# Performance work log

Hardware: AMD Instinct MI355X
Metric: run time of the kernel (lower is better)

## Reference

```python
import jax, jax.numpy as jnp
import numpy as np

B, C, H, W = 8, 512, 32, 32
NH = 8
DH = C // NH
HW = H * W
LN_EPS = 1e-5
NORM_EPS = 1e-12  # torch F.normalize eps


def setup_inputs() -> dict:
    key = jax.random.key(0)
    ks = jax.random.split(key, 8)
    s = 0.02
    return {
        "x": jax.random.normal(ks[0], (B, C, H, W), dtype=jnp.float32),
        "qkv_w": jax.random.normal(ks[1], (3 * C, C), dtype=jnp.float32) * s,
        "proj_w": jax.random.normal(ks[2], (C, C), dtype=jnp.float32) * s,
        "proj_b": jnp.zeros((C,), dtype=jnp.float32),
        "temperature": jnp.ones((NH, 1, 1), dtype=jnp.float32),
        "ln_g": jnp.ones((C,), dtype=jnp.float32),
        "ln_b": jnp.zeros((C,), dtype=jnp.float32),
        "pos_embed": jax.random.normal(ks[3], (1, HW, C), dtype=jnp.float32) * s,
        "dw_w": jax.random.normal(ks[4], (C, 1, 3, 3), dtype=jnp.float32) * s,
        "dw_b": jnp.zeros((C,), dtype=jnp.float32),
        "pw_w": jax.random.normal(ks[5], (C, C, 1, 1), dtype=jnp.float32) * s,
        "pw_b": jnp.zeros((C,), dtype=jnp.float32),
    }


def _l2norm_tokens(t):
    # normalize along token axis (dim=-2), like F.normalize(t, dim=-2)
    n = jnp.sqrt(jnp.sum(t * t, axis=-2, keepdims=True))
    return t / jnp.maximum(n, NORM_EPS)


def _layernorm(t, g, b):
    mu = jnp.mean(t, axis=-1, keepdims=True)
    var = jnp.mean((t - mu) ** 2, axis=-1, keepdims=True)
    return (t - mu) * jax.lax.rsqrt(var + LN_EPS) * g + b


def _dsconv(t, dw_w, dw_b, pw_w, pw_b):
    # depthwise 3x3 SAME + pointwise 1x1, NCHW / OIHW
    y = jax.lax.conv_general_dilated(
        t, dw_w, window_strides=(1, 1), padding="SAME",
        dimension_numbers=("NCHW", "OIHW", "NCHW"), feature_group_count=C)
    y = y + dw_b[None, :, None, None]
    y = jax.lax.conv_general_dilated(
        y, pw_w, window_strides=(1, 1), padding="SAME",
        dimension_numbers=("NCHW", "OIHW", "NCHW"))
    return y + pw_b[None, :, None, None]


def reference(x, qkv_w, proj_w, proj_b, temperature, ln_g, ln_b, pos_embed, dw_w, dw_b, pw_w, pw_b):
    save = x
    t = jnp.transpose(x.reshape(B, C, HW), (0, 2, 1))  # [B, HW, C]
    t = t + pos_embed
    # qkv projection (no bias)
    qkv = t @ qkv_w.T  # [B, HW, 3C]
    qkv = qkv.reshape(B, HW, 3, NH, DH).transpose(2, 0, 3, 1, 4)  # [3,B,NH,HW,DH]
    q, k, v = qkv[0], qkv[1], qkv[2]
    q = _l2norm_tokens(q)
    k = _l2norm_tokens(k)
    attn = jnp.einsum("bhnd,bhmd->bhnm", q, k) * temperature[None]  # [B,NH,HW,HW]
    attn = jax.nn.softmax(attn, axis=-1)
    o = jnp.einsum("bhnm,bhmd->bhnd", attn, v)  # [B,NH,HW,DH]
    o = o.transpose(0, 2, 1, 3).reshape(B, HW, C)
    o = o @ proj_w.T + proj_b
    o = _layernorm(o, ln_g, ln_b)
    o = jnp.transpose(o, (0, 2, 1)).reshape(B, C, H, W)
    o = o + save
    return o + _dsconv(o, dw_w, dw_b, pw_w, pw_b)
```

## Files before the change

kernel.cpp:

```cpp
#include <hip/hip_runtime.h>
#include <math.h>

#define BB_ 8
#define C_ 512
#define C3_ 1536
#define HW_ 1024
#define NH_ 8
#define DH_ 64
#define HH_ 32
#define WW_ 32

typedef __attribute__((ext_vector_type(8))) short short8;
typedef __attribute__((ext_vector_type(4))) short short4v;
typedef __attribute__((ext_vector_type(8))) unsigned short ushort8;
typedef __attribute__((ext_vector_type(4))) unsigned short ushort4_t;
typedef __attribute__((ext_vector_type(4))) float f32x4;
typedef unsigned short ushort;

__device__ inline ushort f2bf(float f) {
  union { float f; unsigned u; } v;
  v.f = f;
  unsigned r = v.u + 0x7fffu + ((v.u >> 16) & 1u);
  return (ushort)(r >> 16);
}
__device__ inline float bf2f(ushort u) {
  union { unsigned u; float f; } v;
  v.u = ((unsigned)u) << 16;
  return v.f;
}

#define GLD16(gptr, lptr)                                                     \
  __builtin_amdgcn_global_load_lds(                                           \
      (const __attribute__((address_space(1))) unsigned int*)(gptr),          \
      (__attribute__((address_space(3))) unsigned int*)(lptr), 16, 0, 0)

__device__ inline f32x4 pv_mfma(short4v vf, short4v pf, f32x4 acc) {
#if __has_builtin(__builtin_amdgcn_mfma_f32_16x16x16_bf16)
  return __builtin_amdgcn_mfma_f32_16x16x16_bf16(vf, pf, acc, 0, 0, 0);
#elif __has_builtin(__builtin_amdgcn_mfma_f32_16x16x16bf16_1k)
  return __builtin_amdgcn_mfma_f32_16x16x16bf16_1k(vf, pf, acc, 0, 0, 0);
#else
  short8 vf8 = {vf[0], vf[1], vf[2], vf[3], 0, 0, 0, 0};
  short8 pf8 = {pf[0], pf[1], pf[2], pf[3], 0, 0, 0, 0};
  return __builtin_amdgcn_mfma_f32_16x16x32_bf16(vf8, pf8, acc, 0, 0, 0);
#endif
}

__global__ __launch_bounds__(256) void prep_kernel(
    const float* __restrict__ x, const float* __restrict__ pos,
    const float* __restrict__ qkv_w, const float* __restrict__ proj_w,
    const float* __restrict__ pw_w, ushort* __restrict__ t,
    ushort* __restrict__ xT, ushort* __restrict__ wts,
    float* __restrict__ sums) {
  const int bid = blockIdx.x;
  const int tid = threadIdx.x;
  if (bid >= 6144) {
    sums[(bid - 6144) * 256 + tid] = 0.f;
    return;
  }
  if (bid >= 1024) {
    int i = (bid - 1024) * 256 + tid;
    if (i < 786432) wts[i] = f2bf(qkv_w[i]);
    else if (i < 1048576) wts[i] = f2bf(proj_w[i - 786432]);
    else wts[i] = f2bf(pw_w[i - 1048576]);
    return;
  }
  __shared__ float tile[64][65];
  const int n0 = (bid & 15) * 64, c0 = ((bid >> 4) & 7) * 64, b = bid >> 7;
#pragma unroll
  for (int it = 0; it < 4; it++) {
    int c_l = (tid >> 4) + it * 16;
    int n_l4 = (tid & 15) * 4;
    float4 v = *(const float4*)&x[((size_t)(b * C_ + c0 + c_l)) * HW_ + n0 + n_l4];
    tile[c_l][n_l4 + 0] = v.x;
    tile[c_l][n_l4 + 1] = v.y;
    tile[c_l][n_l4 + 2] = v.z;
    tile[c_l][n_l4 + 3] = v.w;
  }
  __syncthreads();
#pragma unroll
  for (int it = 0; it < 4; it++) {
    int n_l = (tid >> 4) + it * 16;
    int c_l4 = (tid & 15) * 4;
    size_t token = (size_t)(b * HW_ + n0 + n_l);
    float4 pv = *(const float4*)&pos[(n0 + n_l) * C_ + c0 + c_l4];
    float xv0 = tile[c_l4 + 0][n_l], xv1 = tile[c_l4 + 1][n_l];
    float xv2 = tile[c_l4 + 2][n_l], xv3 = tile[c_l4 + 3][n_l];
    ushort4_t tb = {f2bf(xv0 + pv.x), f2bf(xv1 + pv.y), f2bf(xv2 + pv.z),
                    f2bf(xv3 + pv.w)};
    ushort4_t xb = {f2bf(xv0), f2bf(xv1), f2bf(xv2), f2bf(xv3)};
    *(ushort4_t*)&t[token * C_ + c0 + c_l4] = tb;
    *(ushort4_t*)&xT[token * C_ + c0 + c_l4] = xb;
  }
}

__global__ __launch_bounds__(256) void gemm_qkv(
    const ushort* __restrict__ A, const ushort* __restrict__ Wm,
    ushort* __restrict__ out, ushort* __restrict__ vt,
    float* __restrict__ qsum, float* __restrict__ ksum) {
  const int N = C3_, K = C_;
  __shared__ alignas(16) ushort As[128 * 32];
  __shared__ alignas(16) ushort Bs[128 * 32];
  const int bn = blockIdx.x * 128, bm = blockIdx.y * 128;
  const int tid = threadIdx.x;
  const int w = tid >> 6, lane = tid & 63;
  const int wm = 64 * (w & 1), wn = 64 * (w >> 1);
  const int l15 = lane & 15, lq = lane >> 4;

  f32x4 acc[4][4];
#pragma unroll
  for (int i = 0; i < 4; i++)
#pragma unroll
    for (int j = 0; j < 4; j++) acc[i][j] = (f32x4){0.f, 0.f, 0.f, 0.f};

  const int srr = lane >> 2, sq1 = lane & 3;

  for (int k0 = 0; k0 < K; k0 += 32) {
    __syncthreads();
#pragma unroll
    for (int j = 0; j < 2; j++) {
      int r = 32 * w + 16 * j + srr;
      int q = (sq1 - (r >> 1)) & 3;
      GLD16(A + (size_t)(bm + r) * K + k0 + q * 8, &As[(32 * w + 16 * j) * 32]);
      GLD16(Wm + (size_t)(bn + r) * K + k0 + q * 8, &Bs[(32 * w + 16 * j) * 32]);
    }
    __syncthreads();
    short8 af[4], bf[4];
#pragma unroll
    for (int nt = 0; nt < 4; nt++) {
      int r = wm + nt * 16 + l15;
      af[nt] = *(const short8*)&As[r * 32 + (((lq + (r >> 1)) & 3) * 8)];
      int c = wn + nt * 16 + l15;
      bf[nt] = *(const short8*)&Bs[c * 32 + (((lq + (c >> 1)) & 3) * 8)];
    }
#pragma unroll
    for (int i = 0; i < 4; i++)
#pragma unroll
      for (int j = 0; j < 4; j++)
        acc[i][j] = __builtin_amdgcn_mfma_f32_16x16x32_bf16(af[i], bf[j],
                                                            acc[i][j], 0, 0, 0);
  }

  const int b = bm >> 10;
  if (bn < 1024) {
#pragma unroll
    for (int j = 0; j < 4; j++) {
      int c = bn + wn + j * 16 + l15;
      float ss = 0.f;
#pragma unroll
      for (int i = 0; i < 4; i++) {
#pragma unroll
        for (int r = 0; r < 4; r++) {
          int m = bm + wm + i * 16 + lq * 4 + r;
          float v = acc[i][j][r];
          ss += v * v;
          out[(size_t)m * N + c] = f2bf(v);
        }
      }
      ss += __shfl_xor(ss, 16);
      ss += __shfl_xor(ss, 32);
      if (lq == 0) {
        if (c < 512) atomicAdd(&qsum[b * 512 + c], ss);
        else atomicAdd(&ksum[b * 512 + c - 512], ss);
      }
    }
  } else {
#pragma unroll
    for (int j = 0; j < 4; j++) {
      int c = bn + wn + j * 16 + l15;
      int hd = c - 1024;
      ushort* vrow = vt + ((size_t)(b * 512 + hd)) * HW_;
#pragma unroll
      for (int i = 0; i < 4; i++) {
        int n0 = (bm & 1023) + wm + i * 16 + lq * 4;
        ushort4_t pv = {f2bf(acc[i][j][0]), f2bf(acc[i][j][1]),
                        f2bf(acc[i][j][2]), f2bf(acc[i][j][3])};
        *(ushort4_t*)&vrow[n0] = pv;
      }
    }
  }
}

template <int EPI>
__global__ __launch_bounds__(256) void gemm_n64(
    const ushort* __restrict__ A, const ushort* __restrict__ Wm,
    const float* __restrict__ bias, void* __restrict__ outv,
    const ushort* __restrict__ resid, int N, int K) {
  __shared__ alignas(16) ushort As[128 * 32];
  __shared__ alignas(16) ushort Bs[64 * 32];
  const int bn = blockIdx.x * 64, bm = blockIdx.y * 128;
  const int tid = threadIdx.x;
  const int w = tid >> 6, lane = tid & 63;
  const int wm = 64 * (w & 1), wn = 32 * (w >> 1);
  const int l15 = lane & 15, lq = lane >> 4;

  f32x4 acc[4][2];
#pragma unroll
  for (int i = 0; i < 4; i++)
#pragma unroll
    for (int j = 0; j < 2; j++) acc[i][j] = (f32x4){0.f, 0.f, 0.f, 0.f};

  const int srr = lane >> 2, sq1 = lane & 3;

  for (int k0 = 0; k0 < K; k0 += 32) {
    __syncthreads();
#pragma unroll
    for (int j = 0; j < 2; j++) {
      int r = 32 * w + 16 * j + srr;
      int q = (sq1 - (r >> 1)) & 3;
      GLD16(A + (size_t)(bm + r) * K + k0 + q * 8, &As[(32 * w + 16 * j) * 32]);
    }
    {
      int r = 16 * w + srr;
      int q = (sq1 - (r >> 1)) & 3;
      GLD16(Wm + (size_t)(bn + r) * K + k0 + q * 8, &Bs[(16 * w) * 32]);
    }
    __syncthreads();
    short8 af[4], bf[2];
#pragma unroll
    for (int nt = 0; nt < 4; nt++) {
      int r = wm + nt * 16 + l15;
      af[nt] = *(const short8*)&As[r * 32 + (((lq + (r >> 1)) & 3) * 8)];
    }
#pragma unroll
    for (int j = 0; j < 2; j++) {
      int c = wn + j * 16 + l15;
      bf[j] = *(const short8*)&Bs[c * 32 + (((lq + (c >> 1)) & 3) * 8)];
    }
#pragma unroll
    for (int i = 0; i < 4; i++)
#pragma unroll
      for (int j = 0; j < 2; j++)
        acc[i][j] = __builtin_amdgcn_mfma_f32_16x16x32_bf16(af[i], bf[j],
                                                            acc[i][j], 0, 0, 0);
  }

#pragma unroll
  for (int i = 0; i < 4; i++) {
#pragma unroll
    for (int j = 0; j < 2; j++) {
      int c = bn + wn + j * 16 + l15;
      float bv = bias[c];
#pragma unroll
      for (int r = 0; r < 4; r++) {
        int m = bm + wm + i * 16 + lq * 4 + r;
        float v = acc[i][j][r] + bv;
        if (EPI == 1) {
          ((ushort*)outv)[(size_t)m * N + c] = f2bf(v);
        } else {
          int b = m >> 10, s = m & (HW_ - 1);
          ((float*)outv)[((size_t)(b * C_ + c)) * HW_ + s] =
              v + bf2f(resid[(size_t)m * C_ + c]);
        }
      }
    }
  }
}

__global__ __launch_bounds__(256) void attn_mfma_kernel(
    const ushort* __restrict__ qkv, const ushort* __restrict__ vt,
    const float* __restrict__ qsum, const float* __restrict__ ksum,
    const float* __restrict__ temp, ushort* __restrict__ o) {
  __shared__ alignas(16) ushort Ks[2][64 * 64];
  __shared__ alignas(16) ushort Vts[2][64 * 64];
  __shared__ float sc_lds[64];

  const int tid = threadIdx.x;
  const int w = tid >> 6, lane = tid & 63;
  const int quad = lane >> 4, lcol = lane & 15;
  const int bh = blockIdx.x & 63;
  const int qt = blockIdx.x >> 6;
  const int b = bh >> 3, h = bh & 7;
  const int q0 = qt * 128;

  if (tid < 64) {
    float qs = qsum[b * 512 + h * 64 + tid];
    float ks = ksum[b * 512 + h * 64 + tid];
    float iq = 1.0f / fmaxf(sqrtf(qs), 1e-12f);
    float ik = 1.0f / fmaxf(sqrtf(ks), 1e-12f);
    sc_lds[tid] = iq * ik * temp[h];
  }

  const ushort* kg = qkv + (size_t)b * HW_ * C3_ + C_ + h * 64;
  const ushort* vg = vt + (size_t)(bh * 64) * HW_;

  const int srow0 = tid >> 3;
  const int sc = tid & 7;

#pragma unroll
  for (int it = 0; it < 2; it++) {
    int row = srow0 + it * 32;
    int scg = sc ^ (row & 7);
    GLD16(kg + (size_t)row * C3_ + scg * 8, &Ks[0][w * 512 + it * 2048]);
    GLD16(vg + (size_t)row * HW_ + scg * 8, &Vts[0][w * 512 + it * 2048]);
  }
  __syncthreads();

  short8 qf[2][2];
#pragma unroll
  for (int qg = 0; qg < 2; qg++) {
    const int m = q0 + w * 32 + qg * 16 + lcol;
    const ushort* qrow = qkv + ((size_t)(b * HW_ + m)) * C3_ + h * 64;
#pragma unroll
    for (int kc = 0; kc < 2; kc++) {
      union { short8 v; ushort u[8]; } pk;
#pragma unroll
      for (int j = 0; j < 8; j++) {
        int d = kc * 32 + quad * 8 + j;
        pk.u[j] = f2bf(bf2f(qrow[d]) * sc_lds[d]);
      }
      qf[qg][kc] = pk.v;
    }
  }

  f32x4 ot[2][4];
#pragma unroll
  for (int qg = 0; qg < 2; qg++)
#pragma unroll
    for (int dt = 0; dt < 4; dt++) ot[qg][dt] = (f32x4){0.f, 0.f, 0.f, 0.f};
  float lsum[2] = {0.f, 0.f};

  for (int kt = 0; kt < 16; kt++) {
    if (kt > 0) __syncthreads();
    const int cur = kt & 1;
    if (kt + 1 < 16) {
      const int nxt = cur ^ 1;
#pragma unroll
      for (int it = 0; it < 2; it++) {
        int row = srow0 + it * 32;
        int scg = sc ^ (row & 7);
        GLD16(kg + (size_t)((kt + 1) * 64 + row) * C3_ + scg * 8,
              &Ks[nxt][w * 512 + it * 2048]);
        GLD16(vg + (size_t)row * HW_ + (kt + 1) * 64 + scg * 8,
              &Vts[nxt][w * 512 + it * 2048]);
      }
    }

    f32x4 sfr[2][4];
#pragma unroll
    for (int qg = 0; qg < 2; qg++)
#pragma unroll
      for (int nt = 0; nt < 4; nt++) sfr[qg][nt] = (f32x4){0.f, 0.f, 0.f, 0.f};
#pragma unroll
    for (int kc = 0; kc < 2; kc++) {
#pragma unroll
      for (int nt = 0; nt < 4; nt++) {
        int row = nt * 16 + lcol;
        short8 kf = *(const short8*)
            &Ks[cur][row * 64 + (((kc * 4 + quad) ^ (row & 7)) * 8)];
        sfr[0][nt] = __builtin_amdgcn_mfma_f32_16x16x32_bf16(kf, qf[0][kc],
                                                             sfr[0][nt], 0, 0, 0);
        sfr[1][nt] = __builtin_amdgcn_mfma_f32_16x16x32_bf16(kf, qf[1][kc],
                                                             sfr[1][nt], 0, 0, 0);
      }
    }

    short4v pk[2][4];
#pragma unroll
    for (int qg = 0; qg < 2; qg++) {
#pragma unroll
      for (int nt = 0; nt < 4; nt++) {
        float f0 = __expf(sfr[qg][nt][0]);
        float f1 = __expf(sfr[qg][nt][1]);
        float f2 = __expf(sfr[qg][nt][2]);
        float f3 = __expf(sfr[qg][nt][3]);
        lsum[qg] += f0 + f1 + f2 + f3;
        pk[qg][nt] = (short4v){(short)f2bf(f0), (short)f2bf(f1),
                               (short)f2bf(f2), (short)f2bf(f3)};
      }
    }

#pragma unroll
    for (int nt = 0; nt < 4; nt++) {
      int key = nt * 16 + quad * 4;
#pragma unroll
      for (int dt = 0; dt < 4; dt++) {
        int d = dt * 16 + lcol;
        short4v vf = *(const short4v*)
            &Vts[cur][d * 64 + (((key >> 3) ^ (d & 7)) * 8) + (key & 7)];
        ot[0][dt] = pv_mfma(vf, pk[0][nt], ot[0][dt]);
        ot[1][dt] = pv_mfma(vf, pk[1][nt], ot[1][dt]);
      }
    }
  }

#pragma unroll
  for (int qg = 0; qg < 2; qg++) {
    float s = lsum[qg];
    s += __shfl_xor(s, 16);
    s += __shfl_xor(s, 32);
    const float inv = 1.0f / s;
    const int m = q0 + w * 32 + qg * 16 + lcol;
    ushort* orow = o + ((size_t)(b * HW_ + m)) * C_ + h * 64;
#pragma unroll
    for (int dt = 0; dt < 4; dt++) {
      ushort4_t pkb = {f2bf(ot[qg][dt][0] * inv), f2bf(ot[qg][dt][1] * inv),
                       f2bf(ot[qg][dt][2] * inv), f2bf(ot[qg][dt][3] * inv)};
      *(ushort4_t*)&orow[dt * 16 + quad * 4] = pkb;
    }
  }
}

__global__ __launch_bounds__(256) void ln_residual_kernel(
    const ushort* __restrict__ po, const ushort* xT,
    const float* __restrict__ g, const float* __restrict__ bb, ushort* ybf) {
  const int wv = threadIdx.x >> 6, lane = threadIdx.x & 63;
  const int token = blockIdx.x * 4 + wv;
  const int c0 = lane * 8;
  ushort8 p8 = *(const ushort8*)&po[(size_t)token * C_ + c0];
  float v[8];
  float s = 0.f;
#pragma unroll
  for (int j = 0; j < 8; j++) {
    v[j] = bf2f(p8[j]);
    s += v[j];
  }
#pragma unroll
  for (int off = 32; off; off >>= 1) s += __shfl_xor(s, off);
  float mu = s * (1.0f / C_);
  float vs = 0.f;
#pragma unroll
  for (int j = 0; j < 8; j++) {
    v[j] -= mu;
    vs += v[j] * v[j];
  }
#pragma unroll
  for (int off = 32; off; off >>= 1) vs += __shfl_xor(vs, off);
  float rstd = rsqrtf(vs * (1.0f / C_) + 1e-5f);
  float4 g0 = *(const float4*)&g[c0], g1 = *(const float4*)&g[c0 + 4];
  float4 b0 = *(const float4*)&bb[c0], b1 = *(const float4*)&bb[c0 + 4];
  ushort8 r8 = *(const ushort8*)&xT[(size_t)token * C_ + c0];
  float gg[8] = {g0.x, g0.y, g0.z, g0.w, g1.x, g1.y, g1.z, g1.w};
  float bbv[8] = {b0.x, b0.y, b0.z, b0.w, b1.x, b1.y, b1.z, b1.w};
  ushort8 pk;
#pragma unroll
  for (int j = 0; j < 8; j++)
    pk[j] = f2bf(v[j] * rstd * gg[j] + bbv[j] + bf2f(r8[j]));
  *(ushort8*)&ybf[(size_t)token * C_ + c0] = pk;
}

__global__ __launch_bounds__(256) void dwconv_kernel(
    const ushort* __restrict__ y, const float* __restrict__ w,
    const float* __restrict__ bias, ushort* __restrict__ out) {
  const int cg = threadIdx.x & 63, tg = threadIdx.x >> 6;
  const int c0 = cg * 8;
  float wreg[9][8], breg[8];
#pragma unroll
  for (int j = 0; j < 8; j++) {
    breg[j] = bias[c0 + j];
#pragma unroll
    for (int kk = 0; kk < 9; kk++) wreg[kk][j] = w[(c0 + j) * 9 + kk];
  }
  for (int i = 0; i < 4; i++) {
    int token = blockIdx.x * 16 + tg * 4 + i;
    int b = token >> 10, s = token & (HW_ - 1);
    int hh = s >> 5, ww = s & 31;
    float acc[8];
#pragma unroll
    for (int j = 0; j < 8; j++) acc[j] = breg[j];
#pragma unroll
    for (int ky = 0; ky < 3; ky++) {
      int yy = hh + ky - 1;
      if (yy < 0 || yy >= HH_) continue;
#pragma unroll
      for (int kx = 0; kx < 3; kx++) {
        int xx = ww + kx - 1;
        if (xx < 0 || xx >= WW_) continue;
        ushort8 v8 = *(const ushort8*)
            &y[((size_t)(b * HW_ + yy * 32 + xx)) * C_ + c0];
        const float* wk = wreg[ky * 3 + kx];
#pragma unroll
        for (int j = 0; j < 8; j++) acc[j] += wk[j] * bf2f(v8[j]);
      }
    }
    ushort8 pk;
#pragma unroll
    for (int j = 0; j < 8; j++) pk[j] = f2bf(acc[j]);
    *(ushort8*)&out[(size_t)token * C_ + c0] = pk;
  }
}

extern "C" void kernel_launch(void* const* d_in, const int* in_sizes, int n_in,
                              void* d_out, int out_size, void* d_ws,
                              size_t ws_size, hipStream_t stream) {
  const float* x = (const float*)d_in[0];
  const float* qkv_w = (const float*)d_in[1];
  const float* proj_w = (const float*)d_in[2];
  const float* proj_b = (const float*)d_in[3];
  const float* temperature = (const float*)d_in[4];
  const float* ln_g = (const float*)d_in[5];
  const float* ln_b = (const float*)d_in[6];
  const float* pos = (const float*)d_in[7];
  const float* dw_w = (const float*)d_in[8];
  const float* dw_b = (const float*)d_in[9];
  const float* pw_w = (const float*)d_in[10];
  const float* pw_b = (const float*)d_in[11];
  float* out = (float*)d_out;

  float* ws = (float*)d_ws;
  ushort* qkv_bf = (ushort*)ws;
  ushort* t_bf = (ushort*)(ws + (size_t)6 * 1024 * 1024);
  ushort* proj_bf = (ushort*)(ws + (size_t)8 * 1024 * 1024);
  ushort* xT_bf = (ushort*)(ws + (size_t)12 * 1024 * 1024);
  ushort* wts = (ushort*)(ws + (size_t)14 * 1024 * 1024);
  ushort* qkvw_bf = wts;
  ushort* projw_bf = wts + 786432;
  ushort* pww_bf = wts + 1048576;
  float* sums = ws + (size_t)15 * 1024 * 1024;
  float* qsum = sums;
  float* ksum = sums + 4096;
  ushort* vtb = (ushort*)(ws + (size_t)16 * 1024 * 1024);

  const int M = BB_ * HW_;

  prep_kernel<<<6176, 256, 0, stream>>>(x, pos, qkv_w, proj_w, pw_w, t_bf,
                                        xT_bf, wts, sums);
  gemm_qkv<<<dim3(C3_ / 128, M / 128), 256, 0, stream>>>(
      t_bf, qkvw_bf, qkv_bf, vtb, qsum, ksum);
  attn_mfma_kernel<<<BB_ * NH_ * (HW_ / 128), 256, 0, stream>>>(
      qkv_bf, vtb, qsum, ksum, temperature, t_bf);
  gemm_n64<1><<<dim3(C_ / 64, M / 128), 256, 0, stream>>>(
      t_bf, projw_bf, proj_b, proj_bf, nullptr, C_, C_);
  ln_residual_kernel<<<M / 4, 256, 0, stream>>>(proj_bf, xT_bf, ln_g, ln_b,
                                                xT_bf);
  dwconv_kernel<<<M / 16, 256, 0, stream>>>(xT_bf, dw_w, dw_b, t_bf);
  gemm_n64<2><<<dim3(C_ / 64, M / 128), 256, 0, stream>>>(
      t_bf, pww_bf, pw_b, out, xT_bf, C_, C_);
}
```

Baseline: 208.9 us.

## Stage transposed GEMM epilogue through LDS; use exp2 and vector Q loads in attention

The EPI==2 GEMM epilogue previously wrote fp32 outputs to NCHW with a scattered, strided store per element. It now stages the tile in a swizzled LDS buffer and writes coalesced 16-byte rows. The attention kernel folds log2(e) into the Q scale so it can use the hardware exp2 instead of __expf, and loads Q rows as 8-wide vectors. The extra 32KB of LDS in the EPI==2 variant may lower occupancy.

```diff
diff --git a/kernel.cpp b/kernel.cpp
--- a/kernel.cpp
+++ b/kernel.cpp
@@ -27,6 +27,14 @@
   union { unsigned u; float f; } v;
   v.u = ((unsigned)u) << 16;
   return v.f;
+}
+
+__device__ inline float fast_exp2(float x) {
+#if __has_builtin(__builtin_amdgcn_exp2f)
+  return __builtin_amdgcn_exp2f(x);
+#else
+  return exp2f(x);
+#endif
 }
 
 #define GLD16(gptr, lptr)                                                     \
@@ -188,6 +196,7 @@
     const ushort* __restrict__ resid, int N, int K) {
   __shared__ alignas(16) ushort As[128 * 32];
   __shared__ alignas(16) ushort Bs[64 * 32];
+  __shared__ alignas(16) float Cs[EPI == 2 ? 64 * 128 : 4];
   const int bn = blockIdx.x * 64, bm = blockIdx.y * 128;
   const int tid = threadIdx.x;
   const int w = tid >> 6, lane = tid & 63;
@@ -235,24 +244,50 @@
                                                             acc[i][j], 0, 0, 0);
   }
 
-#pragma unroll
-  for (int i = 0; i < 4; i++) {
-#pragma unroll
-    for (int j = 0; j < 2; j++) {
-      int c = bn + wn + j * 16 + l15;
-      float bv = bias[c];
-#pragma unroll
-      for (int r = 0; r < 4; r++) {
-        int m = bm + wm + i * 16 + lq * 4 + r;
-        float v = acc[i][j][r] + bv;
-        if (EPI == 1) {
+  if (EPI == 1) {
+#pragma unroll
+    for (int i = 0; i < 4; i++) {
+#pragma unroll
+      for (int j = 0; j < 2; j++) {
+        int c = bn + wn + j * 16 + l15;
+        float bv = bias[c];
+#pragma unroll
+        for (int r = 0; r < 4; r++) {
+          int m = bm + wm + i * 16 + lq * 4 + r;
+          float v = acc[i][j][r] + bv;
           ((ushort*)outv)[(size_t)m * N + c] = f2bf(v);
-        } else {
-          int b = m >> 10, s = m & (HW_ - 1);
-          ((float*)outv)[((size_t)(b * C_ + c)) * HW_ + s] =
-              v + bf2f(resid[(size_t)m * C_ + c]);
         }
       }
+    }
+  } else {
+#pragma unroll
+    for (int i = 0; i < 4; i++) {
+#pragma unroll
+      for (int j = 0; j < 2; j++) {
+        int c_l = wn + j * 16 + l15;
+        int m_l = wm + i * 16 + lq * 4;
+        float bv = bias[bn + c_l];
+        f32x4 vv;
+#pragma unroll
+        for (int r = 0; r < 4; r++) {
+          int m = bm + m_l + r;
+          vv[r] = acc[i][j][r] + bv + bf2f(resid[(size_t)m * C_ + bn + c_l]);
+        }
+        int phys = (m_l >> 2) ^ (c_l & 31);
+        *(f32x4*)&Cs[c_l * 128 + phys * 4] = vv;
+      }
+    }
+    __syncthreads();
+    const int b = bm >> 10, s0 = bm & (HW_ - 1);
+    const int l5 = tid & 31;
+    const int rr = tid >> 5;
+    float* outp = (float*)outv;
+#pragma unroll
+    for (int pass = 0; pass < 8; pass++) {
+      int row = rr + pass * 8;
+      int phys = l5 ^ (row & 31);
+      f32x4 vv = *(const f32x4*)&Cs[row * 128 + phys * 4];
+      *(f32x4*)&outp[((size_t)(b * C_ + bn + row)) * HW_ + s0 + l5 * 4] = vv;
     }
   }
 }
@@ -278,7 +313,7 @@
     float ks = ksum[b * 512 + h * 64 + tid];
     float iq = 1.0f / fmaxf(sqrtf(qs), 1e-12f);
     float ik = 1.0f / fmaxf(sqrtf(ks), 1e-12f);
-    sc_lds[tid] = iq * ik * temp[h];
+    sc_lds[tid] = iq * ik * temp[h] * 1.44269504088896340736f;
   }
 
   const ushort* kg = qkv + (size_t)b * HW_ * C3_ + C_ + h * 64;
@@ -303,11 +338,12 @@
     const ushort* qrow = qkv + ((size_t)(b * HW_ + m)) * C3_ + h * 64;
 #pragma unroll
     for (int kc = 0; kc < 2; kc++) {
+      ushort8 q8 = *(const ushort8*)&qrow[kc * 32 + quad * 8];
       union { short8 v; ushort u[8]; } pk;
 #pragma unroll
       for (int j = 0; j < 8; j++) {
         int d = kc * 32 + quad * 8 + j;
-        pk.u[j] = f2bf(bf2f(qrow[d]) * sc_lds[d]);
+        pk.u[j] = f2bf(bf2f(q8[j]) * sc_lds[d]);
       }
       qf[qg][kc] = pk.v;
     }
@@ -360,10 +396,10 @@
     for (int qg = 0; qg < 2; qg++) {
 #pragma unroll
       for (int nt = 0; nt < 4; nt++) {
-        float f0 = __expf(sfr[qg][nt][0]);
-        float f1 = __expf(sfr[qg][nt][1]);
-        float f2 = __expf(sfr[qg][nt][2]);
-        float f3 = __expf(sfr[qg][nt][3]);
+        float f0 = fast_exp2(sfr[qg][nt][0]);
+        float f1 = fast_exp2(sfr[qg][nt][1]);
+        float f2 = fast_exp2(sfr[qg][nt][2]);
+        float f3 = fast_exp2(sfr[qg][nt][3]);
         lsum[qg] += f0 + f1 + f2 + f3;
         pk[qg][nt] = (short4v){(short)f2bf(f0), (short)f2bf(f1),
                                (short)f2bf(f2), (short)f2bf(f3)};
```

Result: faster. 200.2 us (-4.2%).
